# Optimization experiments

Hardware: AMD Instinct MI355X
Metric: run time of the kernel (lower is better)

Reference implementation:

```python
import jax, jax.numpy as jnp
import numpy as np

D_MODEL = 1024
N_HEADS = 16
D_K = 64
CHUNK_LEN = 64


def setup_inputs() -> dict:
    key = jax.random.key(0)
    ks = jax.random.split(key, 10)
    B, S = 4, 2048
    NC, NN, NL = 32, 2, 128
    s = 1.0 / np.sqrt(D_MODEL)
    inp = {
        "query": jax.random.normal(ks[0], (B, S, D_MODEL), dtype=jnp.float32),
        "key": jax.random.normal(ks[1], (B, NC, NN, NL, D_MODEL), dtype=jnp.float32),
        # Linear weights stored as [in, out] (equivalent to torch W.T)
        "Wq": jax.random.normal(ks[2], (D_MODEL, N_HEADS * D_K), dtype=jnp.float32) * s,
        "bq": jnp.zeros((N_HEADS * D_K,), dtype=jnp.float32),
        "Wk": jax.random.normal(ks[3], (D_MODEL, N_HEADS * D_K), dtype=jnp.float32) * s,
        "bk": jnp.zeros((N_HEADS * D_K,), dtype=jnp.float32),
        "Wv": jax.random.normal(ks[4], (D_MODEL, N_HEADS * D_K), dtype=jnp.float32) * s,
        "bv": jnp.zeros((N_HEADS * D_K,), dtype=jnp.float32),
        "Wo": jax.random.normal(ks[5], (N_HEADS * D_K, D_MODEL), dtype=jnp.float32) * s,
        "bo": jnp.zeros((D_MODEL,), dtype=jnp.float32),
    }
    return inp


def reference(query, key, Wq, bq, Wk, bk, Wv, bv, Wo, bo):
    B, S, D = query.shape
    _, NC, NN, NL, _ = key.shape
    L = NN * NL  # kv length per chunk
    # reshape query into chunks: [B, NC, chunk_len, D]
    q_in = query.reshape(B, NC, CHUNK_LEN, D)
    kv_in = key.reshape(B, NC, L, D)  # key used for both K and V in the original
    # projections, split heads: [B, NC, H, T, d_k]
    q = (q_in @ Wq + bq).reshape(B, NC, CHUNK_LEN, N_HEADS, D_K).transpose(0, 1, 3, 2, 4)
    k = (kv_in @ Wk + bk).reshape(B, NC, L, N_HEADS, D_K).transpose(0, 1, 3, 2, 4)
    v = (kv_in @ Wv + bv).reshape(B, NC, L, N_HEADS, D_K).transpose(0, 1, 3, 2, 4)
    # attention per (batch, chunk, head)
    scores = jnp.einsum("bchqd,bchkd->bchqk", q, k) / jnp.sqrt(jnp.float32(D_K))
    attn = jax.nn.softmax(scores, axis=-1)
    o = jnp.einsum("bchqk,bchkd->bchqd", attn, v)
    # merge heads: [B, NC, chunk_len, H*d_k]
    o = o.transpose(0, 1, 3, 2, 4).reshape(B, NC, CHUNK_LEN, N_HEADS * D_K)
    out = o @ Wo + bo
    return out.reshape(B, S, D)
```

## Files before the change

kernel.cpp:

```cpp
#include <hip/hip_runtime.h>
#include <hip/hip_bf16.h>
#include <stdint.h>

#define DMODEL 1024
#define NHEADS 16
#define DK 64
#define TQ 64
#define LKV 256
#define MQ 8192
#define MKV 32768

typedef __bf16 bf16x8 __attribute__((ext_vector_type(8)));
typedef float f32x4 __attribute__((ext_vector_type(4)));
typedef unsigned short u16x8 __attribute__((ext_vector_type(8)));
typedef unsigned short u16;

__device__ __forceinline__ unsigned short f2bf(float f) {
    union { float f; unsigned int i; } x; x.f = f;
    unsigned int r = (x.i + 0x7FFFu + ((x.i >> 16) & 1u)) >> 16;
    return (unsigned short)r;
}

__device__ __forceinline__ void gload_lds16(const void* g, void* l) {
    __builtin_amdgcn_global_load_lds(
        (const __attribute__((address_space(1))) unsigned int*)g,
        (__attribute__((address_space(3))) unsigned int*)l, 16, 0, 0);
}

__global__ __launch_bounds__(256) void cvt_f32_bf16(const float* __restrict__ in,
                                                    unsigned short* __restrict__ out) {
    long long i = ((long long)blockIdx.x * 256 + threadIdx.x) * 8;
    f32x4 a = *(const f32x4*)(in + i);
    f32x4 b = *(const f32x4*)(in + i + 4);
    u16x8 o;
    o[0] = f2bf(a[0]); o[1] = f2bf(a[1]); o[2] = f2bf(a[2]); o[3] = f2bf(a[3]);
    o[4] = f2bf(b[0]); o[5] = f2bf(b[1]); o[6] = f2bf(b[2]); o[7] = f2bf(b[3]);
    *(u16x8*)(out + i) = o;
}

__global__ __launch_bounds__(256) void transpose_w_cvt4(const float* __restrict__ w0,
                                                        const float* __restrict__ w1,
                                                        const float* __restrict__ w2,
                                                        const float* __restrict__ w3,
                                                        u16* __restrict__ o0,
                                                        u16* __restrict__ o1,
                                                        u16* __restrict__ o2,
                                                        u16* __restrict__ o3) {
    __shared__ float tile[64][65];
    const float* in; u16* out;
    switch (blockIdx.z) {
        case 0: in = w0; out = o0; break;
        case 1: in = w1; out = o1; break;
        case 2: in = w2; out = o2; break;
        default: in = w3; out = o3; break;
    }
    int bi = blockIdx.y, bj = blockIdx.x;
    int tid = threadIdx.x;
    int c = tid & 63, r0 = tid >> 6;
#pragma unroll
    for (int p = 0; p < 16; ++p) {
        int r = r0 + 4 * p;
        tile[r][c] = in[(size_t)(bi * 64 + r) * 1024 + bj * 64 + c];
    }
    __syncthreads();
#pragma unroll
    for (int p = 0; p < 16; ++p) {
        int r = r0 + 4 * p;
        out[(size_t)(bj * 64 + r) * 1024 + bi * 64 + c] = f2bf(tile[c][r]);
    }
}

template <int OUTMODE>
__global__ __launch_bounds__(256) void gemm_bias(const u16* __restrict__ A,
                                                 const u16* __restrict__ Bt,
                                                 const float* __restrict__ bias,
                                                 void* __restrict__ OutV) {
    __shared__ alignas(16) u16 aLds[128 * 32];
    __shared__ alignas(16) u16 bLds[128 * 32];

    int tid = threadIdx.x;
    int lane = tid & 63, wid = tid >> 6;
    int m0 = blockIdx.x * 128;
    int n0 = blockIdx.y * 128;
    int wr = (wid >> 1) * 64, wc = (wid & 1) * 64;

    f32x4 zero = {0.f, 0.f, 0.f, 0.f};
    f32x4 acc[4][4];
#pragma unroll
    for (int i = 0; i < 4; ++i)
#pragma unroll
        for (int j = 0; j < 4; ++j) acc[i][j] = zero;

    int sr = lane >> 2;
    int sk = (lane & 3) * 8;
    const u16* aG = A + (size_t)(m0 + sr) * 1024 + sk;
    const u16* bG = Bt + (size_t)(n0 + sr) * 1024 + sk;
    int c0 = wid, c1 = wid + 4;

    int fr = lane & 15, fg = (lane >> 4) * 8;

    for (int kt = 0; kt < 1024; kt += 32) {
        gload_lds16(aG + (size_t)(c0 * 16) * 1024 + kt, aLds + c0 * 512);
        gload_lds16(aG + (size_t)(c1 * 16) * 1024 + kt, aLds + c1 * 512);
        gload_lds16(bG + (size_t)(c0 * 16) * 1024 + kt, bLds + c0 * 512);
        gload_lds16(bG + (size_t)(c1 * 16) * 1024 + kt, bLds + c1 * 512);
        __syncthreads();

        bf16x8 af[4], bf[4];
#pragma unroll
        for (int mt = 0; mt < 4; ++mt)
            af[mt] = *(const bf16x8*)&aLds[(wr + mt * 16 + fr) * 32 + fg];
#pragma unroll
        for (int nt = 0; nt < 4; ++nt)
            bf[nt] = *(const bf16x8*)&bLds[(wc + nt * 16 + fr) * 32 + fg];
#pragma unroll
        for (int mt = 0; mt < 4; ++mt)
#pragma unroll
            for (int nt = 0; nt < 4; ++nt)
                acc[mt][nt] = __builtin_amdgcn_mfma_f32_16x16x32_bf16(af[mt], bf[nt], acc[mt][nt], 0, 0, 0);
        __syncthreads();
    }

    float bv[4];
#pragma unroll
    for (int nt = 0; nt < 4; ++nt) bv[nt] = bias[n0 + wc + nt * 16 + fr];

    if (OUTMODE == 0) {
        u16* Out = (u16*)OutV;
#pragma unroll
        for (int mt = 0; mt < 4; ++mt)
#pragma unroll
            for (int r = 0; r < 4; ++r) {
                size_t row = (size_t)(m0 + wr + mt * 16 + (lane >> 4) * 4 + r);
#pragma unroll
                for (int nt = 0; nt < 4; ++nt)
                    Out[row * 1024 + n0 + wc + nt * 16 + fr] = f2bf(acc[mt][nt][r] + bv[nt]);
            }
    } else {
        float* Out = (float*)OutV;
#pragma unroll
        for (int mt = 0; mt < 4; ++mt)
#pragma unroll
            for (int r = 0; r < 4; ++r) {
                size_t row = (size_t)(m0 + wr + mt * 16 + (lane >> 4) * 4 + r);
#pragma unroll
                for (int nt = 0; nt < 4; ++nt)
                    Out[row * 1024 + n0 + wc + nt * 16 + fr] = acc[mt][nt][r] + bv[nt];
            }
    }
}


__device__ __forceinline__ void stage64(const u16* src, u16* ldsTile, int row0, int tid) {
    int w = tid >> 6, l = tid & 63;
    int r = row0 + w * 8 + (l >> 3);
    int k16 = (l & 7) ^ ((l >> 3) & 7);
    gload_lds16(src + (size_t)r * 1024 + k16 * 8, ldsTile + (size_t)(row0 + w * 8) * 64);
}

#define SBAR() do { __builtin_amdgcn_s_barrier(); asm volatile("" ::: "memory"); } while (0)

__global__ __launch_bounds__(512, 2) void proj_fused(const u16* __restrict__ Akv,
                                                     const u16* __restrict__ Aq,
                                                     const u16* __restrict__ WkT,
                                                     const u16* __restrict__ WvT,
                                                     const u16* __restrict__ WqT,
                                                     const float* __restrict__ bk,
                                                     const float* __restrict__ bv,
                                                     const float* __restrict__ bq,
                                                     u16* __restrict__ Kp,
                                                     u16* __restrict__ Vt,
                                                     u16* __restrict__ Qp,
                                                     int nmKV, int nmQ) {
    __shared__ alignas(16) u16 lds[81920];
    u16* ldsA0 = lds;
    u16* ldsA1 = lds + 16384;
    u16* ldsB  = lds + 32768;

    int tid = threadIdx.x, lane = tid & 63, wid = tid >> 6;
    int wm = wid >> 2, wn = wid & 3;

    int nB = gridDim.x;
    int bid = blockIdx.x;
    int qq = nB >> 3, rr = nB & 7;
    int xcd = bid & 7, idx = bid >> 3;
    int wg = (xcd < rr) ? xcd * (qq + 1) + idx : rr * (qq + 1) + (xcd - rr) * qq + idx;

    const u16* A; const u16* B; const float* bias; u16* Out; int mode;
    int nKV4 = nmKV * 4;
    int lwg;
    if (wg < nKV4)            { lwg = wg;            A = Akv; B = WkT; bias = bk; Out = Kp; mode = 0; }
    else if (wg < 2 * nKV4)   { lwg = wg - nKV4;     A = Akv; B = WvT; bias = bv; Out = Vt; mode = 1; }
    else                      { lwg = wg - 2 * nKV4; A = Aq;  B = WqT; bias = bq; Out = Qp; mode = 0; }
    int m0 = (lwg >> 2) * 256;
    int n0 = (lwg & 3) * 256;

    const u16* aSrc = A + (size_t)m0 * 1024;
    const u16* bSrc = B + (size_t)n0 * 1024;

    f32x4 zero = {0.f, 0.f, 0.f, 0.f};
    f32x4 acc[8][4];
#pragma unroll
    for (int i = 0; i < 8; ++i)
#pragma unroll
        for (int j = 0; j < 4; ++j) acc[i][j] = zero;

    bf16x8 aR[4][2], b0R[2][2], b1R[2][2];

#define READ_A(lA, half)                                                         \
    do {                                                                         \
        _Pragma("unroll") for (int mf = 0; mf < 4; ++mf) {                       \
            int row = wm * 128 + (half) * 64 + mf * 16 + (lane & 15);            \
            _Pragma("unroll") for (int kk = 0; kk < 2; ++kk) {                   \
                int k16 = kk * 4 + (lane >> 4);                                  \
                aR[mf][kk] = *(const bf16x8*)&(lA)[row * 64 + ((k16 ^ (row & 7)) << 3)]; \
            }                                                                    \
        }                                                                        \
    } while (0)
#define READ_B(lB, half, dst)                                                    \
    do {                                                                         \
        _Pragma("unroll") for (int nf = 0; nf < 2; ++nf) {                       \
            int row = wn * 64 + (half) * 32 + nf * 16 + (lane & 15);             \
            _Pragma("unroll") for (int kk = 0; kk < 2; ++kk) {                   \
                int k16 = kk * 4 + (lane >> 4);                                  \
                dst[nf][kk] = *(const bf16x8*)&(lB)[row * 64 + ((k16 ^ (row & 7)) << 3)]; \
            }                                                                    \
        }                                                                        \
    } while (0)
#define MFMA16(mh, nh, bR)                                                       \
    do {                                                                         \
        __builtin_amdgcn_s_setprio(1);                                           \
        _Pragma("unroll") for (int mf = 0; mf < 4; ++mf)                         \
            _Pragma("unroll") for (int nf = 0; nf < 2; ++nf)                     \
                _Pragma("unroll") for (int kk = 0; kk < 2; ++kk)                 \
                    acc[(mh)*4 + mf][(nh)*2 + nf] =                              \
                        __builtin_amdgcn_mfma_f32_16x16x32_bf16(                 \
                            aR[mf][kk], bR[nf][kk], acc[(mh)*4 + mf][(nh)*2 + nf], 0, 0, 0); \
        __builtin_amdgcn_s_setprio(0);                                           \
    } while (0)

    stage64(bSrc, ldsB, 0, tid);          stage64(bSrc, ldsB, 64, tid);
    stage64(bSrc, ldsB, 128, tid);        stage64(bSrc, ldsB, 192, tid);
    stage64(aSrc, ldsA0, 0, tid);         stage64(aSrc, ldsA0, 64, tid);
    stage64(aSrc, ldsA0, 128, tid);       stage64(aSrc, ldsA0, 192, tid);
    stage64(bSrc + 64, ldsB + 16384, 0, tid);   stage64(bSrc + 64, ldsB + 16384, 64, tid);
    stage64(bSrc + 64, ldsB + 16384, 128, tid); stage64(bSrc + 64, ldsB + 16384, 192, tid);
    asm volatile("s_waitcnt vmcnt(4)" ::: "memory");
    SBAR();

    int bi = 0;
    for (int t = 0; t < 16; ++t) {
        u16* lA = (t & 1) ? ldsA1 : ldsA0;
        u16* lB = ldsB + bi * 16384;
        u16* pA = (t & 1) ? ldsA0 : ldsA1;
        int bi2 = bi + 2; if (bi2 >= 3) bi2 -= 3;
        u16* pB = ldsB + bi2 * 16384;
        const u16* aN = aSrc + (t + 1) * 64;
        const u16* bN2 = bSrc + (t + 2) * 64;
        bool pfA = (t < 15), pfB = (t < 14);

        READ_A(lA, 0);
        READ_B(lB, 0, b0R);
        if (pfA) { stage64(aN, pA, 0, tid); stage64(aN, pA, 128, tid); }
        MFMA16(0, 0, b0R);

        READ_B(lB, 1, b1R);
        if (pfA) { stage64(aN, pA, 64, tid); stage64(aN, pA, 192, tid); }
        MFMA16(0, 1, b1R);

        READ_A(lA, 1);
        if (pfB) { stage64(bN2, pB, 0, tid); stage64(bN2, pB, 64, tid); }
        MFMA16(1, 1, b1R);

        if (pfB) { stage64(bN2, pB, 128, tid); stage64(bN2, pB, 192, tid); }
        MFMA16(1, 0, b0R);

        if (t < 14)      { asm volatile("s_waitcnt vmcnt(4)" ::: "memory"); SBAR(); }
        else if (t == 14){ asm volatile("s_waitcnt vmcnt(0)" ::: "memory"); SBAR(); }

        bi = bi + 1; if (bi >= 3) bi -= 3;
    }

    float bvv[4];
#pragma unroll
    for (int NF = 0; NF < 4; ++NF) bvv[NF] = bias[n0 + wn * 64 + NF * 16 + (lane & 15)];

    if (mode == 0) {
#pragma unroll
        for (int MF = 0; MF < 8; ++MF)
#pragma unroll
            for (int r = 0; r < 4; ++r) {
                size_t row = (size_t)(m0 + wm * 128 + MF * 16 + (lane >> 4) * 4 + r);
#pragma unroll
                for (int NF = 0; NF < 4; ++NF)
                    Out[row * 1024 + n0 + wn * 64 + NF * 16 + (lane & 15)] =
                        f2bf(acc[MF][NF][r] + bvv[NF]);
            }
    } else {
#pragma unroll
        for (int MF = 0; MF < 8; ++MF)
#pragma unroll
            for (int r = 0; r < 4; ++r) {
                int gm = m0 + wm * 128 + MF * 16 + (lane >> 4) * 4 + r;
                int bc2 = gm >> 8, lv = gm & 255;
#pragma unroll
                for (int NF = 0; NF < 4; ++NF) {
                    int n = n0 + wn * 64 + NF * 16 + (lane & 15);
                    int hh = n >> 6, dd = n & 63;
                    Out[(size_t)((bc2 * 16 + hh) * 64 + dd) * 256 + lv] =
                        f2bf(acc[MF][NF][r] + bvv[NF]);
                }
            }
    }
#undef READ_A
#undef READ_B
#undef MFMA16
}

__global__ __launch_bounds__(256) void attn_kernel(const u16* __restrict__ Q,
                                                   const u16* __restrict__ K,
                                                   const u16* __restrict__ Vt,
                                                   u16* O) {
    __shared__ alignas(16) u16 pLds[64 * 264];

    int tid = threadIdx.x;
    int lane = tid & 63, w = tid >> 6;
    int bc = blockIdx.x >> 4, h = blockIdx.x & 15;
    int fr = lane & 15, g = lane >> 4;

    const u16* qb = Q + (size_t)(bc * 64 + w * 16 + fr) * 1024 + h * 64 + g * 8;
    bf16x8 qf0 = *(const bf16x8*)qb;
    bf16x8 qf1 = *(const bf16x8*)(qb + 32);

    const u16* kb = K + (size_t)(bc * 256 + fr) * 1024 + h * 64 + g * 8;

    f32x4 zero = {0.f, 0.f, 0.f, 0.f};
    f32x4 sc[16];
#pragma unroll
    for (int nt = 0; nt < 16; ++nt) sc[nt] = zero;

#pragma unroll
    for (int nt = 0; nt < 16; ++nt) {
        bf16x8 kf0 = *(const bf16x8*)(kb + (size_t)(nt * 16) * 1024);
        bf16x8 kf1 = *(const bf16x8*)(kb + (size_t)(nt * 16) * 1024 + 32);
        sc[nt] = __builtin_amdgcn_mfma_f32_16x16x32_bf16(qf0, kf0, sc[nt], 0, 0, 0);
        sc[nt] = __builtin_amdgcn_mfma_f32_16x16x32_bf16(qf1, kf1, sc[nt], 0, 0, 0);
    }

    const float scale = 0.125f;
    float mx[4], sum[4];
#pragma unroll
    for (int r = 0; r < 4; ++r) {
        float m = -1e30f;
#pragma unroll
        for (int nt = 0; nt < 16; ++nt) {
            sc[nt][r] *= scale;
            m = fmaxf(m, sc[nt][r]);
        }
#pragma unroll
        for (int x = 1; x < 16; x <<= 1) m = fmaxf(m, __shfl_xor(m, x, 64));
        mx[r] = m;
        sum[r] = 0.f;
    }
#pragma unroll
    for (int nt = 0; nt < 16; ++nt)
#pragma unroll
        for (int r = 0; r < 4; ++r) {
            float p = __expf(sc[nt][r] - mx[r]);
            sum[r] += p;
            pLds[(w * 16 + g * 4 + r) * 264 + nt * 16 + fr] = f2bf(p);
        }
#pragma unroll
    for (int r = 0; r < 4; ++r)
#pragma unroll
        for (int x = 1; x < 16; x <<= 1) sum[r] += __shfl_xor(sum[r], x, 64);

    __syncthreads();

    f32x4 oa[4];
#pragma unroll
    for (int nt = 0; nt < 4; ++nt) oa[nt] = zero;

    const u16* vtb = Vt + (size_t)((bc * 16 + h) * 64) * 256;
#pragma unroll
    for (int ks = 0; ks < 8; ++ks) {
        bf16x8 pf = *(const bf16x8*)&pLds[(w * 16 + fr) * 264 + ks * 32 + g * 8];
#pragma unroll
        for (int nt = 0; nt < 4; ++nt) {
            bf16x8 vf = *(const bf16x8*)(vtb + (size_t)(nt * 16 + fr) * 256 + ks * 32 + g * 8);
            oa[nt] = __builtin_amdgcn_mfma_f32_16x16x32_bf16(pf, vf, oa[nt], 0, 0, 0);
        }
    }

    float rs[4];
#pragma unroll
    for (int r = 0; r < 4; ++r) rs[r] = 1.0f / sum[r];

    u16* ob = O + (size_t)(bc * 64 + w * 16 + g * 4) * 1024 + h * 64 + fr;
#pragma unroll
    for (int nt = 0; nt < 4; ++nt)
#pragma unroll
        for (int r = 0; r < 4; ++r)
            ob[(size_t)r * 1024 + nt * 16] = f2bf(oa[nt][r] * rs[r]);
}

extern "C" void kernel_launch(void* const* d_in, const int* in_sizes, int n_in,
                              void* d_out, int out_size, void* d_ws, size_t ws_size,
                              hipStream_t stream) {
    const float* query = (const float*)d_in[0];
    const float* keyin = (const float*)d_in[1];
    const float* Wq = (const float*)d_in[2];
    const float* bq = (const float*)d_in[3];
    const float* Wk = (const float*)d_in[4];
    const float* bk = (const float*)d_in[5];
    const float* Wv = (const float*)d_in[6];
    const float* bv = (const float*)d_in[7];
    const float* Wo = (const float*)d_in[8];
    const float* bo = (const float*)d_in[9];

    u16* ws = (u16*)d_ws;
    const size_t MB1 = 1024 * 1024;

    u16* WqT = ws;
    u16* WkT = ws + MB1;
    u16* WvT = ws + 2 * MB1;
    u16* WoT = ws + 3 * MB1;
    u16* qb16 = ws + 4 * MB1;
    u16* Qp   = qb16 + (size_t)MQ * 1024;
    u16* kvb  = Qp + (size_t)MQ * 1024;

    size_t ws_elems = ws_size / 2;
    size_t fixed = 4 * MB1 + 2 * (size_t)MQ * 1024;
    size_t avail = (ws_elems > fixed) ? (ws_elems - fixed) : 0;
    long long max_rows = (long long)(avail / (3 * 1024));
    int slice_rows = (int)((max_rows / 1024) * 1024);
    if (slice_rows >= MKV) slice_rows = MKV;
    else if (slice_rows >= 16384) slice_rows = 16384;
    if (slice_rows < 1024) slice_rows = 1024;

    u16* Kp = kvb + (size_t)slice_rows * 1024;
    u16* Vt = Kp + (size_t)slice_rows * 1024;

    dim3 tb(256);
    transpose_w_cvt4<<<dim3(16, 16, 4), tb, 0, stream>>>(Wq, Wk, Wv, Wo, WqT, WkT, WvT, WoT);
    cvt_f32_bf16<<<dim3(MQ * 1024 / (256 * 8)), tb, 0, stream>>>(query, qb16);

    int qdone = 0;
    for (int r0 = 0; r0 < MKV; r0 += slice_rows) {
        int rows = MKV - r0;
        if (rows > slice_rows) rows = slice_rows;
        cvt_f32_bf16<<<dim3(rows * 1024 / (256 * 8)), tb, 0, stream>>>(
            keyin + (size_t)r0 * 1024, kvb);
        int nmKV = rows / 256;
        int nmQ = rows / 1024;
        proj_fused<<<dim3(nmKV * 8 + nmQ * 4), dim3(512), 0, stream>>>(
            kvb, qb16 + (size_t)qdone * 256 * 1024,
            WkT, WvT, WqT, bk, bv, bq,
            Kp, Vt, Qp + (size_t)qdone * 256 * 1024, nmKV, nmQ);
        size_t qoff = (size_t)(r0 / 4) * 1024;
        attn_kernel<<<dim3((rows / 256) * 16), tb, 0, stream>>>(
            Qp + qoff, Kp, Vt, Qp + qoff);
        qdone += nmQ;
    }

    gemm_bias<2><<<dim3(MQ / 128, 8), tb, 0, stream>>>(Qp, WoT, bo, d_out);
}
```

Before: 316.3 us.

## Shrink projection GEMM tiles to 128x256 with BK=32 double buffering

Rewrites the fused projection kernel to use 128x256 output tiles and a 32-wide K step, with simple A/B double buffering in place of the triple-buffered B with staggered prefetch. LDS use drops sharply and launch bounds allow 4 blocks per CU, so occupancy rises. The cost is a full vmcnt(0) wait plus a barrier every K step, twice as many steps, and more redundant B-tile loads. Attention blocks are also remapped across XCDs for locality.

New measurement: 331.1 us. +4.7%, slower.

```diff
diff --git a/kernel.cpp b/kernel.cpp
--- a/kernel.cpp
+++ b/kernel.cpp
@@ -151,16 +151,16 @@
 }
 
 
-__device__ __forceinline__ void stage64(const u16* src, u16* ldsTile, int row0, int tid) {
-    int w = tid >> 6, l = tid & 63;
-    int r = row0 + w * 8 + (l >> 3);
-    int k16 = (l & 7) ^ ((l >> 3) & 7);
-    gload_lds16(src + (size_t)r * 1024 + k16 * 8, ldsTile + (size_t)(row0 + w * 8) * 64);
+__device__ __forceinline__ void stage128(const u16* src, u16* ldsDst, int tid) {
+    int l = tid & 63;
+    int row = tid >> 2;
+    int slot = (l & 3) ^ ((l >> 3) & 3);
+    gload_lds16(src + (size_t)row * 1024 + slot * 8, ldsDst + (size_t)(tid >> 6) * 512);
 }
 
 #define SBAR() do { __builtin_amdgcn_s_barrier(); asm volatile("" ::: "memory"); } while (0)
 
-__global__ __launch_bounds__(512, 2) void proj_fused(const u16* __restrict__ Akv,
+__global__ __launch_bounds__(512, 4) void proj_fused(const u16* __restrict__ Akv,
                                                      const u16* __restrict__ Aq,
                                                      const u16* __restrict__ WkT,
                                                      const u16* __restrict__ WvT,
@@ -172,13 +172,13 @@
                                                      u16* __restrict__ Vt,
                                                      u16* __restrict__ Qp,
                                                      int nmKV, int nmQ) {
-    __shared__ alignas(16) u16 lds[81920];
-    u16* ldsA0 = lds;
-    u16* ldsA1 = lds + 16384;
-    u16* ldsB  = lds + 32768;
+    __shared__ alignas(16) u16 lds[24576];
+    u16* ldsA0 = lds;          u16* ldsA1 = lds + 4096;
+    u16* ldsB0 = lds + 8192;   u16* ldsB1 = lds + 16384;
 
     int tid = threadIdx.x, lane = tid & 63, wid = tid >> 6;
     int wm = wid >> 2, wn = wid & 3;
+    int fr = lane & 15, g = lane >> 4;
 
     int nB = gridDim.x;
     int bid = blockIdx.x;
@@ -192,128 +192,101 @@
     if (wg < nKV4)            { lwg = wg;            A = Akv; B = WkT; bias = bk; Out = Kp; mode = 0; }
     else if (wg < 2 * nKV4)   { lwg = wg - nKV4;     A = Akv; B = WvT; bias = bv; Out = Vt; mode = 1; }
     else                      { lwg = wg - 2 * nKV4; A = Aq;  B = WqT; bias = bq; Out = Qp; mode = 0; }
-    int m0 = (lwg >> 2) * 256;
+    int m0 = (lwg >> 2) * 128;
     int n0 = (lwg & 3) * 256;
 
     const u16* aSrc = A + (size_t)m0 * 1024;
     const u16* bSrc = B + (size_t)n0 * 1024;
+    const u16* bSrc2 = bSrc + (size_t)128 * 1024;
 
     f32x4 zero = {0.f, 0.f, 0.f, 0.f};
-    f32x4 acc[8][4];
-#pragma unroll
-    for (int i = 0; i < 8; ++i)
+    f32x4 acc[4][4];
+#pragma unroll
+    for (int i = 0; i < 4; ++i)
 #pragma unroll
         for (int j = 0; j < 4; ++j) acc[i][j] = zero;
 
-    bf16x8 aR[4][2], b0R[2][2], b1R[2][2];
-
-#define READ_A(lA, half)                                                         \
+    bf16x8 aF[4], bF[4];
+
+#define LADDR(row) ((row) * 32 + (((g ^ (((row) >> 1) & 3))) << 3))
+#define READ_AB(lA, lB)                                                          \
     do {                                                                         \
         _Pragma("unroll") for (int mf = 0; mf < 4; ++mf) {                       \
-            int row = wm * 128 + (half) * 64 + mf * 16 + (lane & 15);            \
-            _Pragma("unroll") for (int kk = 0; kk < 2; ++kk) {                   \
-                int k16 = kk * 4 + (lane >> 4);                                  \
-                aR[mf][kk] = *(const bf16x8*)&(lA)[row * 64 + ((k16 ^ (row & 7)) << 3)]; \
-            }                                                                    \
+            int row = wm * 64 + mf * 16 + fr;                                    \
+            aF[mf] = *(const bf16x8*)&(lA)[LADDR(row)];                          \
+        }                                                                        \
+        _Pragma("unroll") for (int nf = 0; nf < 4; ++nf) {                       \
+            int row = wn * 64 + nf * 16 + fr;                                    \
+            bF[nf] = *(const bf16x8*)&(lB)[LADDR(row)];                          \
         }                                                                        \
     } while (0)
-#define READ_B(lB, half, dst)                                                    \
-    do {                                                                         \
-        _Pragma("unroll") for (int nf = 0; nf < 2; ++nf) {                       \
-            int row = wn * 64 + (half) * 32 + nf * 16 + (lane & 15);             \
-            _Pragma("unroll") for (int kk = 0; kk < 2; ++kk) {                   \
-                int k16 = kk * 4 + (lane >> 4);                                  \
-                dst[nf][kk] = *(const bf16x8*)&(lB)[row * 64 + ((k16 ^ (row & 7)) << 3)]; \
-            }                                                                    \
-        }                                                                        \
-    } while (0)
-#define MFMA16(mh, nh, bR)                                                       \
+#define MFMA16()                                                                 \
     do {                                                                         \
         __builtin_amdgcn_s_setprio(1);                                           \
         _Pragma("unroll") for (int mf = 0; mf < 4; ++mf)                         \
-            _Pragma("unroll") for (int nf = 0; nf < 2; ++nf)                     \
-                _Pragma("unroll") for (int kk = 0; kk < 2; ++kk)                 \
-                    acc[(mh)*4 + mf][(nh)*2 + nf] =                              \
-                        __builtin_amdgcn_mfma_f32_16x16x32_bf16(                 \
-                            aR[mf][kk], bR[nf][kk], acc[(mh)*4 + mf][(nh)*2 + nf], 0, 0, 0); \
+            _Pragma("unroll") for (int nf = 0; nf < 4; ++nf)                     \
+                acc[mf][nf] = __builtin_amdgcn_mfma_f32_16x16x32_bf16(           \
+                    aF[mf], bF[nf], acc[mf][nf], 0, 0, 0);                       \
         __builtin_amdgcn_s_setprio(0);                                           \
     } while (0)
 
-    stage64(bSrc, ldsB, 0, tid);          stage64(bSrc, ldsB, 64, tid);
-    stage64(bSrc, ldsB, 128, tid);        stage64(bSrc, ldsB, 192, tid);
-    stage64(aSrc, ldsA0, 0, tid);         stage64(aSrc, ldsA0, 64, tid);
-    stage64(aSrc, ldsA0, 128, tid);       stage64(aSrc, ldsA0, 192, tid);
-    stage64(bSrc + 64, ldsB + 16384, 0, tid);   stage64(bSrc + 64, ldsB + 16384, 64, tid);
-    stage64(bSrc + 64, ldsB + 16384, 128, tid); stage64(bSrc + 64, ldsB + 16384, 192, tid);
-    asm volatile("s_waitcnt vmcnt(4)" ::: "memory");
+    stage128(aSrc, ldsA0, tid);
+    stage128(bSrc, ldsB0, tid);
+    stage128(bSrc2, ldsB0 + 4096, tid);
+    asm volatile("s_waitcnt vmcnt(0)" ::: "memory");
     SBAR();
 
-    int bi = 0;
-    for (int t = 0; t < 16; ++t) {
+    for (int t = 0; t < 32; ++t) {
         u16* lA = (t & 1) ? ldsA1 : ldsA0;
-        u16* lB = ldsB + bi * 16384;
+        u16* lB = (t & 1) ? ldsB1 : ldsB0;
         u16* pA = (t & 1) ? ldsA0 : ldsA1;
-        int bi2 = bi + 2; if (bi2 >= 3) bi2 -= 3;
-        u16* pB = ldsB + bi2 * 16384;
-        const u16* aN = aSrc + (t + 1) * 64;
-        const u16* bN2 = bSrc + (t + 2) * 64;
-        bool pfA = (t < 15), pfB = (t < 14);
-
-        READ_A(lA, 0);
-        READ_B(lB, 0, b0R);
-        if (pfA) { stage64(aN, pA, 0, tid); stage64(aN, pA, 128, tid); }
-        MFMA16(0, 0, b0R);
-
-        READ_B(lB, 1, b1R);
-        if (pfA) { stage64(aN, pA, 64, tid); stage64(aN, pA, 192, tid); }
-        MFMA16(0, 1, b1R);
-
-        READ_A(lA, 1);
-        if (pfB) { stage64(bN2, pB, 0, tid); stage64(bN2, pB, 64, tid); }
-        MFMA16(1, 1, b1R);
-
-        if (pfB) { stage64(bN2, pB, 128, tid); stage64(bN2, pB, 192, tid); }
-        MFMA16(1, 0, b0R);
-
-        if (t < 14)      { asm volatile("s_waitcnt vmcnt(4)" ::: "memory"); SBAR(); }
-        else if (t == 14){ asm volatile("s_waitcnt vmcnt(0)" ::: "memory"); SBAR(); }
-
-        bi = bi + 1; if (bi >= 3) bi -= 3;
+        u16* pB = (t & 1) ? ldsB0 : ldsB1;
+        bool pf = (t < 31);
+
+        READ_AB(lA, lB);
+        if (pf) {
+            stage128(aSrc + (t + 1) * 32, pA, tid);
+            stage128(bSrc + (t + 1) * 32, pB, tid);
+            stage128(bSrc2 + (t + 1) * 32, pB + 4096, tid);
+        }
+        MFMA16();
+        asm volatile("s_waitcnt vmcnt(0)" ::: "memory");
+        SBAR();
     }
 
     float bvv[4];
 #pragma unroll
-    for (int NF = 0; NF < 4; ++NF) bvv[NF] = bias[n0 + wn * 64 + NF * 16 + (lane & 15)];
+    for (int NF = 0; NF < 4; ++NF) bvv[NF] = bias[n0 + wn * 64 + NF * 16 + fr];
 
     if (mode == 0) {
 #pragma unroll
-        for (int MF = 0; MF < 8; ++MF)
+        for (int MF = 0; MF < 4; ++MF)
 #pragma unroll
             for (int r = 0; r < 4; ++r) {
-                size_t row = (size_t)(m0 + wm * 128 + MF * 16 + (lane >> 4) * 4 + r);
+                size_t row = (size_t)(m0 + wm * 64 + MF * 16 + (lane >> 4) * 4 + r);
 #pragma unroll
                 for (int NF = 0; NF < 4; ++NF)
-                    Out[row * 1024 + n0 + wn * 64 + NF * 16 + (lane & 15)] =
+                    Out[row * 1024 + n0 + wn * 64 + NF * 16 + fr] =
                         f2bf(acc[MF][NF][r] + bvv[NF]);
             }
     } else {
 #pragma unroll
-        for (int MF = 0; MF < 8; ++MF)
+        for (int MF = 0; MF < 4; ++MF)
 #pragma unroll
             for (int r = 0; r < 4; ++r) {
-                int gm = m0 + wm * 128 + MF * 16 + (lane >> 4) * 4 + r;
+                int gm = m0 + wm * 64 + MF * 16 + (lane >> 4) * 4 + r;
                 int bc2 = gm >> 8, lv = gm & 255;
 #pragma unroll
                 for (int NF = 0; NF < 4; ++NF) {
-                    int n = n0 + wn * 64 + NF * 16 + (lane & 15);
+                    int n = n0 + wn * 64 + NF * 16 + fr;
                     int hh = n >> 6, dd = n & 63;
                     Out[(size_t)((bc2 * 16 + hh) * 64 + dd) * 256 + lv] =
                         f2bf(acc[MF][NF][r] + bvv[NF]);
                 }
             }
     }
-#undef READ_A
-#undef READ_B
+#undef LADDR
+#undef READ_AB
 #undef MFMA16
 }
 
@@ -325,7 +298,9 @@
 
     int tid = threadIdx.x;
     int lane = tid & 63, w = tid >> 6;
-    int bc = blockIdx.x >> 4, h = blockIdx.x & 15;
+    int nBl = gridDim.x;
+    int wk = (blockIdx.x & 7) * (nBl >> 3) + (blockIdx.x >> 3);
+    int bc = wk >> 4, h = wk & 15;
     int fr = lane & 15, g = lane >> 4;
 
     const u16* qb = Q + (size_t)(bc * 64 + w * 16 + fr) * 1024 + h * 64 + g * 8;
@@ -451,12 +426,12 @@
         if (rows > slice_rows) rows = slice_rows;
         cvt_f32_bf16<<<dim3(rows * 1024 / (256 * 8)), tb, 0, stream>>>(
             keyin + (size_t)r0 * 1024, kvb);
-        int nmKV = rows / 256;
-        int nmQ = rows / 1024;
-        proj_fused<<<dim3(nmKV * 8 + nmQ * 4), dim3(512), 0, stream>>>(
-            kvb, qb16 + (size_t)qdone * 256 * 1024,
+        int nmKV = rows / 128;
+        int nmQ = rows / 512;
+        proj_fused<<<dim3((2 * nmKV + nmQ) * 4), dim3(512), 0, stream>>>(
+            kvb, qb16 + (size_t)qdone * 128 * 1024,
             WkT, WvT, WqT, bk, bv, bq,
-            Kp, Vt, Qp + (size_t)qdone * 256 * 1024, nmKV, nmQ);
+            Kp, Vt, Qp + (size_t)qdone * 128 * 1024, nmKV, nmQ);
         size_t qoff = (size_t)(r0 / 4) * 1024;
         attn_kernel<<<dim3((rows / 256) * 16), tb, 0, stream>>>(
             Qp + qoff, Kp, Vt, Qp + qoff);
```
